# Kernel tuning notes

Hardware: AMD Instinct MI355X
Metric: run time of the kernel (lower is better)

Reference implementation:

```python
import jax, jax.numpy as jnp
import numpy as np

INPUT_NDIMS = 1024
HIDDEN = 512
LATENT = 50
BATCH = 16384

def setup_inputs() -> dict:
    key = jax.random.key(0)
    ks = jax.random.split(key, 12)
    s = 0.02
    x = jax.random.uniform(ks[0], (BATCH, INPUT_NDIMS), dtype=jnp.float32)
    u = 0.01 + 0.98 * jax.random.uniform(ks[1], (BATCH, LATENT), dtype=jnp.float32)
    W1 = s * jax.random.normal(ks[2], (HIDDEN, INPUT_NDIMS), dtype=jnp.float32)
    b1 = jnp.zeros((HIDDEN,), jnp.float32)
    Wa = s * jax.random.normal(ks[3], (LATENT, HIDDEN), dtype=jnp.float32)
    ba = jnp.zeros((LATENT,), jnp.float32)
    Wb = s * jax.random.normal(ks[4], (LATENT, HIDDEN), dtype=jnp.float32)
    bb = jnp.zeros((LATENT,), jnp.float32)
    W2 = s * jax.random.normal(ks[5], (HIDDEN, LATENT), dtype=jnp.float32)
    b2 = jnp.zeros((HIDDEN,), jnp.float32)
    W3 = s * jax.random.normal(ks[6], (INPUT_NDIMS, HIDDEN), dtype=jnp.float32)
    b3 = jnp.zeros((INPUT_NDIMS,), jnp.float32)
    return dict(x=x, u=u, W1=W1, b1=b1, Wa=Wa, ba=ba, Wb=Wb, bb=bb, W2=W2, b2=b2, W3=W3, b3=b3)

def _stick_segments(v):
    # pi[:, k] = v[:, k] * prod_{j<k} (1 - v[:, j])  -- single O(K) cumprod pass
    cp = jnp.cumprod(1.0 - v, axis=1)                       # inclusive cumprod
    excl = jnp.concatenate([jnp.ones_like(cp[:, :1]), cp[:, :-1]], axis=1)
    return v * excl

def reference(x, u, W1, b1, Wa, ba, Wb, bb, W2, b2, W3, b3):
    # encoder: MLP -> positive Kumaraswamy params alpha (param1), beta (param2)
    h = jax.nn.relu(x @ W1.T + b1)                           # [B, H]
    alpha = jax.nn.softplus(h @ Wa.T + ba) + 1e-4            # [B, K]
    beta = jax.nn.softplus(h @ Wb.T + bb) + 1e-4             # [B, K]
    # Kumaraswamy reparameterized sample: v = (1 - u^(1/beta))^(1/alpha)
    v = jnp.power(1.0 - jnp.power(u, 1.0 / beta), 1.0 / alpha)
    # set_v_K_to_one: force last stick fraction to 1 so segments sum to 1
    v = v.at[:, -1].set(1.0)
    pi = _stick_segments(v)                                  # [B, K], rows sum to 1
    # decoder: MLP with sigmoid output
    h2 = jax.nn.relu(pi @ W2.T + b2)                         # [B, H]
    recon = jax.nn.sigmoid(h2 @ W3.T + b3)                   # [B, D]
    return recon, alpha, beta
```

## Files before the change

### kernel.cpp

```cpp
#include <hip/hip_runtime.h>
#include <hip/hip_bf16.h>

typedef __hip_bfloat16 bf16_t;
typedef __attribute__((ext_vector_type(4))) float f32x4;
typedef __attribute__((ext_vector_type(8))) __bf16 bf16x8;
typedef __attribute__((ext_vector_type(8))) short s16x8;
typedef __attribute__((ext_vector_type(4))) unsigned short u16x4;

#define BATCH 16384
#define NDIM  1024
#define HID   512
#define LAT   50

#define LOG2E 1.44269504088896340736f
#define RLOG2E 0.69314718055994530942f

__device__ __forceinline__ float ex2(float x) { return __builtin_amdgcn_exp2f(x); }
__device__ __forceinline__ float lg2(float x) { return __builtin_amdgcn_logf(x); }
__device__ __forceinline__ float rcp(float x) { return __builtin_amdgcn_rcpf(x); }

__device__ inline unsigned short f2b_u(float f) {
  union { bf16_t b; unsigned short u; } cv; cv.b = __float2bfloat16(f); return cv.u;
}

__device__ __forceinline__ void gload16(const void* src, void* dst_lds) {
  __builtin_amdgcn_global_load_lds(
      reinterpret_cast<const __attribute__((address_space(1))) void*>(
          reinterpret_cast<unsigned long long>(src)),
      reinterpret_cast<__attribute__((address_space(3))) void*>(
          static_cast<unsigned>(reinterpret_cast<unsigned long long>(dst_lds))),
      16, 0, 0);
}

#define WAIT_VMCNT(N)                                          \
  do {                                                         \
    asm volatile("s_waitcnt vmcnt(%0)" ::"i"(N) : "memory");   \
    __builtin_amdgcn_sched_barrier(0);                         \
  } while (0)
#define WAIT_LGKM0                                             \
  do {                                                         \
    asm volatile("s_waitcnt lgkmcnt(0)" ::: "memory");         \
    __builtin_amdgcn_sched_barrier(0);                         \
  } while (0)

__global__ void prep_w_kernel(const float* __restrict__ W1, const float* __restrict__ W3,
                              const float* __restrict__ Wa, const float* __restrict__ Wb,
                              const float* __restrict__ W2, const float* __restrict__ ba,
                              const float* __restrict__ bb,
                              bf16_t* __restrict__ w1, bf16_t* __restrict__ w3,
                              bf16_t* __restrict__ wab, bf16_t* __restrict__ w2p,
                              float* __restrict__ bab)
{
  const int W1U  = (HID * NDIM) / 4;
  const int W3U  = (NDIM * HID) / 4;
  const int WABN = 128 * HID;
  const int W2PN = HID * 64;
  const int TOT  = W1U + W3U + WABN + W2PN + 128;
  for (int i = blockIdx.x * blockDim.x + threadIdx.x; i < TOT;
       i += gridDim.x * blockDim.x) {
    int j = i;
    if (j < W1U) {
      const f32x4 v = ((const f32x4*)W1)[j];
      u16x4 o; o[0]=f2b_u(v[0]); o[1]=f2b_u(v[1]); o[2]=f2b_u(v[2]); o[3]=f2b_u(v[3]);
      ((u16x4*)w1)[j] = o; continue;
    }
    j -= W1U;
    if (j < W3U) {
      const f32x4 v = ((const f32x4*)W3)[j];
      u16x4 o; o[0]=f2b_u(v[0]); o[1]=f2b_u(v[1]); o[2]=f2b_u(v[2]); o[3]=f2b_u(v[3]);
      ((u16x4*)w3)[j] = o; continue;
    }
    j -= W3U;
    if (j < WABN) {
      const int n = j >> 9, k = j & 511;
      float v = (n < 50) ? Wa[n * 512 + k] : ((n < 100) ? Wb[(n - 50) * 512 + k] : 0.f);
      wab[j] = __float2bfloat16(v); continue;
    }
    j -= WABN;
    if (j < W2PN) {
      const int n = j >> 6, k = j & 63;
      w2p[j] = __float2bfloat16(k < 50 ? W2[n * 50 + k] : 0.f); continue;
    }
    j -= W2PN;
    bab[j] = (j < 50) ? ba[j] : ((j < 100) ? bb[j - 50] : 0.f);
  }
}

template<int A_F32, int EPI, int BM>
__global__ __launch_bounds__(512, 2)
void gemm8p_kernel(const void* __restrict__ Av, const bf16_t* __restrict__ B,
                   const float* __restrict__ bias, void* __restrict__ out0,
                   int M, int N, int K)
{
  constexpr int BN     = 256;
  constexpr int ABYTES = BM * 128;
  constexpr int BUF    = ABYTES + BN * 128;
  constexpr int MI     = BM / 32;
  constexpr int FPQ    = MI / 4;
  constexpr int RA     = BM / 64;
  constexpr int RB     = 4;
  __shared__ char lds[2 * BUF];

  const int tid  = threadIdx.x;
  const int swzid = ((blockIdx.x & 7) * (gridDim.x >> 3)) + (blockIdx.x >> 3);
  const int nblocks = N / BN;
  const int bn   = swzid % nblocks;
  const int bm   = swzid / nblocks;
  const int wid  = tid >> 6;
  const int lane = tid & 63;
  const int l15  = lane & 15;
  const int l4   = lane >> 4;
  const int wm   = (wid >> 2) * (BM / 2);
  const int wn   = (wid & 3) * 64;
  const int uw   = __builtin_amdgcn_readfirstlane(wid);

  f32x4 acc[MI][4] = {};
  f32x4 areg[4];

  auto stage_A_round = [&](char* buf, int k0, int i) {
    const bf16_t* A = (const bf16_t*)Av;
    const int c  = (i * 8 + uw) * 64 + lane;
    const int r  = c >> 3;
    const int sp = c & 7;
    const int sl = sp ^ (r & 7);
    gload16(A + (size_t)(bm * BM + r) * K + k0 + sl * 8,
            buf + (i * 8 + uw) * 1024);
  };
  auto stage_B_round = [&](char* buf, int k0, int i) {
    char* lB = buf + ABYTES;
    const int c  = (i * 8 + uw) * 64 + lane;
    const int r  = c >> 3;
    const int sp = c & 7;
    const int sl = sp ^ (r & 7);
    gload16(B + (size_t)(bn * BN + r) * K + k0 + sl * 8,
            lB + (i * 8 + uw) * 1024);
  };
  auto load_A_f32 = [&](int k0) {
    const float* A = (const float*)Av;
    #pragma unroll
    for (int j = 0; j < 2; ++j) {
      const int c  = j * 512 + tid;
      const int r  = c >> 3;
      const int sl = c & 7;
      const float* s = A + (size_t)(bm * BM + r) * K + k0 + sl * 8;
      areg[2 * j]     = *(const f32x4*)s;
      areg[2 * j + 1] = *(const f32x4*)(s + 4);
    }
  };
  auto write_A_f32 = [&](char* buf) {
    #pragma unroll
    for (int j = 0; j < 2; ++j) {
      const int c  = j * 512 + tid;
      const int r  = c >> 3;
      const int sl = c & 7;
      const int sp = sl ^ (r & 7);
      union { s16x8 v; unsigned short us[8]; } o;
      const f32x4 v0 = areg[2 * j], v1 = areg[2 * j + 1];
      o.us[0]=f2b_u(v0[0]); o.us[1]=f2b_u(v0[1]); o.us[2]=f2b_u(v0[2]); o.us[3]=f2b_u(v0[3]);
      o.us[4]=f2b_u(v1[0]); o.us[5]=f2b_u(v1[1]); o.us[6]=f2b_u(v1[2]); o.us[7]=f2b_u(v1[3]);
      *(s16x8*)(buf + r * 128 + sp * 16) = o.v;
    }
  };

  const int nt = K >> 6;
  if constexpr (A_F32) {
    load_A_f32(0); write_A_f32(lds);
  } else {
    #pragma unroll
    for (int i = 0; i < RA; ++i) stage_A_round(lds, 0, i);
  }
  #pragma unroll
  for (int i = 0; i < RB; ++i) stage_B_round(lds, 0, i);
  WAIT_VMCNT(0);
  if (A_F32) WAIT_LGKM0;
  __builtin_amdgcn_s_barrier();

  for (int t = 0; t < nt; ++t) {
    char* buf  = lds + (t & 1) * BUF;
    char* nbuf = lds + ((t + 1) & 1) * BUF;
    const char* lA = buf;
    const char* lB = buf + ABYTES;
    const bool pf  = (t + 1 < nt);
    const int k0n  = (t + 1) << 6;

    if (A_F32 && pf) load_A_f32(k0n);

    #pragma unroll
    for (int q = 0; q < 4; ++q) {
      if (pf) {
        if constexpr (A_F32) {
          stage_B_round(nbuf, k0n, q);
        } else {
          if (q < RA) stage_A_round(nbuf, k0n, q);
          stage_B_round(nbuf, k0n, q);
        }
      }
      bf16x8 af[FPQ][2], bfr[4][2];
      #pragma unroll
      for (int f = 0; f < FPQ; ++f)
        #pragma unroll
        for (int h = 0; h < 2; ++h) {
          const int row = wm + (q * FPQ + f) * 16 + l15;
          const int sp  = (h * 4 + l4) ^ (row & 7);
          af[f][h] = *(const bf16x8*)(lA + row * 128 + sp * 16);
        }
      #pragma unroll
      for (int ni = 0; ni < 4; ++ni)
        #pragma unroll
        for (int h = 0; h < 2; ++h) {
          const int row = wn + ni * 16 + l15;
          const int sp  = (h * 4 + l4) ^ (row & 7);
          bfr[ni][h] = *(const bf16x8*)(lB + row * 128 + sp * 16);
        }
      __builtin_amdgcn_s_barrier();
      WAIT_LGKM0;
      __builtin_amdgcn_s_setprio(1);
      #pragma unroll
      for (int f = 0; f < FPQ; ++f)
        #pragma unroll
        for (int ni = 0; ni < 4; ++ni)
          #pragma unroll
          for (int h = 0; h < 2; ++h)
            acc[q * FPQ + f][ni] = __builtin_amdgcn_mfma_f32_16x16x32_bf16(
                af[f][h], bfr[ni][h], acc[q * FPQ + f][ni], 0, 0, 0);
      __builtin_amdgcn_s_setprio(0);
      if (q < 3) __builtin_amdgcn_s_barrier();
    }

    if (A_F32 && pf) write_A_f32(nbuf);
    WAIT_VMCNT(0);
    if (A_F32) WAIT_LGKM0;
    __builtin_amdgcn_s_barrier();
  }

  #pragma unroll
  for (int ni = 0; ni < 4; ++ni) {
    const int n  = bn * BN + wn + ni * 16 + l15;
    const float bv = bias[n];
    #pragma unroll
    for (int mi = 0; mi < MI; ++mi) {
      #pragma unroll
      for (int r = 0; r < 4; ++r) {
        const int m  = bm * BM + wm + mi * 16 + l4 * 4 + r;
        const float t = acc[mi][ni][r] + bv;
        if (EPI == 0) {
          ((bf16_t*)out0)[(size_t)m * N + n] = __float2bfloat16(fmaxf(t, 0.f));
        } else {
          ((float*)out0)[(size_t)m * N + n] = rcp(1.f + ex2(-t * LOG2E));
        }
      }
    }
  }
}

__global__ __launch_bounds__(512, 2)
void abstick_kernel(const bf16_t* __restrict__ A, const bf16_t* __restrict__ wabg,
                    const float* __restrict__ bab, const bf16_t* __restrict__ w2pg,
                    const float* __restrict__ b2, const float* __restrict__ u,
                    float* __restrict__ out_a, float* __restrict__ out_b,
                    bf16_t* __restrict__ h2)
{
  constexpr int BUF = 64 * 128 + 16384;
  constexpr int PIL = 65536;
  constexpr int SMO = 73728;
  __shared__ char lds[100352];

  const int tid  = threadIdx.x;
  const int swzid = ((blockIdx.x & 7) * (gridDim.x >> 3)) + (blockIdx.x >> 3);
  const int bm   = swzid;
  const int wid  = tid >> 6;
  const int lane = tid & 63;
  const int l15  = lane & 15;
  const int l4   = lane >> 4;
  const int wm   = (wid >> 2) * 32;
  const int wn   = (wid & 3) * 32;
  const int uw   = __builtin_amdgcn_readfirstlane(wid);
  const int K    = HID;

  f32x4 acc[2][2] = {};

  auto stage_AB = [&](char* buf, int k0) {
    {
      const int c  = tid;
      const int r  = c >> 3;
      const int sp = c & 7;
      const int sl = sp ^ (r & 7);
      gload16(A + (size_t)(bm * 64 + r) * K + k0 + sl * 8, buf + uw * 1024);
    }
    char* lB = buf + 8192;
    #pragma unroll
    for (int i = 0; i < 2; ++i) {
      const int c  = (i * 8 + uw) * 64 + lane;
      const int r  = c >> 3;
      const int sp = c & 7;
      const int sl = sp ^ (r & 7);
      gload16(wabg + (size_t)r * K + k0 + sl * 8, lB + (i * 8 + uw) * 1024);
    }
  };
  auto compute1 = [&](const char* buf) {
    const char* lA = buf;
    const char* lB = buf + 8192;
    #pragma unroll
    for (int h = 0; h < 2; ++h) {
      bf16x8 af[2], bfr[2];
      #pragma unroll
      for (int mi = 0; mi < 2; ++mi) {
        const int row = wm + mi * 16 + l15;
        const int sp  = (h * 4 + l4) ^ (row & 7);
        af[mi] = *(const bf16x8*)(lA + row * 128 + sp * 16);
      }
      #pragma unroll
      for (int ni = 0; ni < 2; ++ni) {
        const int row = wn + ni * 16 + l15;
        const int sp  = (h * 4 + l4) ^ (row & 7);
        bfr[ni] = *(const bf16x8*)(lB + row * 128 + sp * 16);
      }
      #pragma unroll
      for (int mi = 0; mi < 2; ++mi)
        #pragma unroll
        for (int ni = 0; ni < 2; ++ni)
          acc[mi][ni] = __builtin_amdgcn_mfma_f32_16x16x32_bf16(
              af[mi], bfr[ni], acc[mi][ni], 0, 0, 0);
    }
  };

  stage_AB(lds, 0);
  stage_AB(lds + BUF, 64);
  for (int t = 0; t < 8; ++t) {
    if (t + 1 < 8) WAIT_VMCNT(3);
    else           WAIT_VMCNT(0);
    __builtin_amdgcn_s_barrier();
    compute1(lds + (t & 1) * BUF);
    __builtin_amdgcn_s_barrier();
    __builtin_amdgcn_sched_barrier(0);
    if (t + 2 < 8) stage_AB(lds + (t & 1) * BUF, (t + 2) << 6);
  }

  #pragma unroll
  for (int i = 0; i < 8; ++i) {
    const int c  = (i * 8 + uw) * 64 + lane;
    const int r  = c >> 3;
    const int sp = c & 7;
    const int sl = sp ^ (r & 7);
    gload16(w2pg + (size_t)r * 64 + sl * 8, lds + (i * 8 + uw) * 1024);
  }

  float* sm = (float*)(lds + SMO);
  #pragma unroll
  for (int ni = 0; ni < 2; ++ni) {
    const int n  = wn + ni * 16 + l15;
    const float bv = bab[n];
    #pragma unroll
    for (int mi = 0; mi < 2; ++mi) {
      #pragma unroll
      for (int r = 0; r < 4; ++r) {
        const int ml = wm + mi * 16 + l4 * 4 + r;
        const int m  = bm * 64 + ml;
        const float t = acc[mi][ni][r] + bv;
        if (n < 100) {
          const float y =
              (t > 20.f ? t : lg2(1.f + ex2(t * LOG2E)) * RLOG2E) + 1e-4f;
          if (n < 50) out_a[(size_t)m * 50 + n] = y;
          else        out_b[(size_t)m * 50 + (n - 50)] = y;
          sm[ml * 104 + n + (n < 50 ? 0 : 2)] = y;
        }
      }
    }
  }
  __syncthreads();

  #pragma unroll 1
  for (int rr = 0; rr < 8; ++rr) {
    const int rl = wid * 8 + rr;
    const size_t m = (size_t)(bm * 64 + rl);
    float v = 1.f, t = 1.f;
    if (lane < 49) {
      const float a  = sm[rl * 104 + lane];
      const float b  = sm[rl * 104 + 52 + lane];
      const float uu = u[m * 50 + lane];
      const float tb = ex2(lg2(uu) * rcp(b));
      v = ex2(lg2(1.f - tb) * rcp(a));
      t = 1.f - v;
    }
    float p = t;
    #pragma unroll
    for (int d = 1; d < 64; d <<= 1) {
      const float o = __shfl_up(p, d, 64);
      if (lane >= d) p *= o;
    }
    float e = __shfl_up(p, 1, 64);
    if (lane == 0) e = 1.f;
    const float piv = (lane < 50) ? v * e : 0.f;
    *(unsigned short*)(lds + PIL + rl * 128 +
                       (((lane >> 3) ^ (rl & 7)) << 4) + ((lane & 7) << 1)) =
        f2b_u(piv);
  }
  __syncthreads();

  const int wn3 = (wid & 3) * 128;
  f32x4 acc3[2][8] = {};
  #pragma unroll
  for (int h = 0; h < 2; ++h) {
    bf16x8 af[2], bfr[8];
    #pragma unroll
    for (int mi = 0; mi < 2; ++mi) {
      const int row = wm + mi * 16 + l15;
      const int sp  = (h * 4 + l4) ^ (row & 7);
      af[mi] = *(const bf16x8*)(lds + PIL + row * 128 + sp * 16);
    }
    #pragma unroll
    for (int ni = 0; ni < 8; ++ni) {
      const int row = wn3 + ni * 16 + l15;
      const int sp  = (h * 4 + l4) ^ (row & 7);
      bfr[ni] = *(const bf16x8*)(lds + row * 128 + sp * 16);
    }
    #pragma unroll
    for (int mi = 0; mi < 2; ++mi)
      #pragma unroll
      for (int ni = 0; ni < 8; ++ni)
        acc3[mi][ni] = __builtin_amdgcn_mfma_f32_16x16x32_bf16(
            af[mi], bfr[ni], acc3[mi][ni], 0, 0, 0);
  }
  #pragma unroll
  for (int ni = 0; ni < 8; ++ni) {
    const int n  = wn3 + ni * 16 + l15;
    const float bv = b2[n];
    #pragma unroll
    for (int mi = 0; mi < 2; ++mi) {
      #pragma unroll
      for (int r = 0; r < 4; ++r) {
        const int m  = bm * 64 + wm + mi * 16 + l4 * 4 + r;
        h2[(size_t)m * HID + n] =
            __float2bfloat16(fmaxf(acc3[mi][ni][r] + bv, 0.f));
      }
    }
  }
}

extern "C" void kernel_launch(void* const* d_in, const int* in_sizes, int n_in,
                              void* d_out, int out_size, void* d_ws, size_t ws_size,
                              hipStream_t stream)
{
  const float* x  = (const float*)d_in[0];
  const float* u  = (const float*)d_in[1];
  const float* W1 = (const float*)d_in[2];
  const float* b1 = (const float*)d_in[3];
  const float* Wa = (const float*)d_in[4];
  const float* ba = (const float*)d_in[5];
  const float* Wb = (const float*)d_in[6];
  const float* bb = (const float*)d_in[7];
  const float* W2 = (const float*)d_in[8];
  const float* b2 = (const float*)d_in[9];
  const float* W3 = (const float*)d_in[10];
  const float* b3 = (const float*)d_in[11];

  float* recon  = (float*)d_out;
  float* oalpha = recon + (size_t)BATCH * NDIM;
  float* obeta  = oalpha + (size_t)BATCH * LAT;

  char* ws = (char*)d_ws;
  bf16_t* h2  = (bf16_t*)(ws);
  bf16_t* h   = (bf16_t*)(ws + 16777216);
  bf16_t* w1  = (bf16_t*)(ws + 33554432);
  bf16_t* w3  = (bf16_t*)(ws + 34603008);
  bf16_t* wab = (bf16_t*)(ws + 35651584);
  bf16_t* w2p = (bf16_t*)(ws + 35782656);
  float*  bab = (float*)(ws + 35848192);

  prep_w_kernel<<<512, 256, 0, stream>>>(W1, W3, Wa, Wb, W2, ba, bb,
                                         w1, w3, wab, w2p, bab);
  gemm8p_kernel<1, 0, 128><<<256, 512, 0, stream>>>(
      x, w1, b1, (void*)h, BATCH, HID, NDIM);
  abstick_kernel<<<256, 512, 0, stream>>>(
      h, wab, bab, w2p, b2, u, oalpha, obeta, h2);
  gemm8p_kernel<0, 1, 256><<<256, 512, 0, stream>>>(
      h2, w3, b3, (void*)recon, BATCH, NDIM, HID);
}
```

Measured before the change: 86.60 us.

## Triple-buffer GEMM LDS pipeline, drop intra-tile barriers, fix BM at 128

Both GEMMs now use a three-stage LDS ring that prefetches two k-tiles ahead and waits on a partial vmcnt instead of draining all loads each step. The per-quarter workgroup barriers go away, and B fragments are loaded once per k-tile and reused across the four A sub-tiles. The decoder GEMM now uses BM=128 with twice as many blocks. Launch bounds drop to one block per CU because LDS grows to three buffers, which costs occupancy in exchange for deeper memory latency hiding.

```diff
diff --git a/kernel.cpp b/kernel.cpp
--- a/kernel.cpp
+++ b/kernel.cpp
@@ -86,20 +86,20 @@
   }
 }
 
-template<int A_F32, int EPI, int BM>
-__global__ __launch_bounds__(512, 2)
-void gemm8p_kernel(const void* __restrict__ Av, const bf16_t* __restrict__ B,
+template<int A_F32, int EPI>
+__global__ __launch_bounds__(512, 1)
+void gemm3b_kernel(const void* __restrict__ Av, const bf16_t* __restrict__ B,
                    const float* __restrict__ bias, void* __restrict__ out0,
                    int M, int N, int K)
 {
+  constexpr int BM     = 128;
   constexpr int BN     = 256;
   constexpr int ABYTES = BM * 128;
   constexpr int BUF    = ABYTES + BN * 128;
-  constexpr int MI     = BM / 32;
-  constexpr int FPQ    = MI / 4;
-  constexpr int RA     = BM / 64;
+  constexpr int RA     = 2;
   constexpr int RB     = 4;
-  __shared__ char lds[2 * BUF];
+  constexpr int L      = A_F32 ? RB : (RA + RB);
+  __shared__ char lds[3 * BUF];
 
   const int tid  = threadIdx.x;
   const int swzid = ((blockIdx.x & 7) * (gridDim.x >> 3)) + (blockIdx.x >> 3);
@@ -110,11 +110,11 @@
   const int lane = tid & 63;
   const int l15  = lane & 15;
   const int l4   = lane >> 4;
-  const int wm   = (wid >> 2) * (BM / 2);
+  const int wm   = (wid >> 2) * 64;
   const int wn   = (wid & 3) * 64;
   const int uw   = __builtin_amdgcn_readfirstlane(wid);
 
-  f32x4 acc[MI][4] = {};
+  f32x4 acc[4][4] = {};
   f32x4 areg[4];
 
   auto stage_A_round = [&](char* buf, int k0, int i) {
@@ -171,64 +171,71 @@
   }
   #pragma unroll
   for (int i = 0; i < RB; ++i) stage_B_round(lds, 0, i);
-  WAIT_VMCNT(0);
+  if (nt > 1) {
+    if constexpr (!A_F32) {
+      #pragma unroll
+      for (int i = 0; i < RA; ++i) stage_A_round(lds + BUF, 64, i);
+    }
+    #pragma unroll
+    for (int i = 0; i < RB; ++i) stage_B_round(lds + BUF, 64, i);
+  }
+  WAIT_VMCNT(L);
   if (A_F32) WAIT_LGKM0;
   __builtin_amdgcn_s_barrier();
 
   for (int t = 0; t < nt; ++t) {
-    char* buf  = lds + (t & 1) * BUF;
-    char* nbuf = lds + ((t + 1) & 1) * BUF;
+    char* buf   = lds + (t % 3) * BUF;
+    char* buf1  = lds + ((t + 1) % 3) * BUF;
+    char* buf2  = lds + ((t + 2) % 3) * BUF;
     const char* lA = buf;
     const char* lB = buf + ABYTES;
-    const bool pf  = (t + 1 < nt);
-    const int k0n  = (t + 1) << 6;
-
-    if (A_F32 && pf) load_A_f32(k0n);
+    const bool pf1 = (t + 1 < nt);
+    const bool pf2 = (t + 2 < nt);
+    const int k0n2 = (t + 2) << 6;
+
+    if (A_F32 && pf1) load_A_f32((t + 1) << 6);
+
+    bf16x8 bfr[4][2];
+    #pragma unroll
+    for (int ni = 0; ni < 4; ++ni)
+      #pragma unroll
+      for (int h = 0; h < 2; ++h) {
+        const int row = wn + ni * 16 + l15;
+        const int sp  = (h * 4 + l4) ^ (row & 7);
+        bfr[ni][h] = *(const bf16x8*)(lB + row * 128 + sp * 16);
+      }
 
     #pragma unroll
     for (int q = 0; q < 4; ++q) {
-      if (pf) {
+      if (pf2) {
         if constexpr (A_F32) {
-          stage_B_round(nbuf, k0n, q);
+          stage_B_round(buf2, k0n2, q);
         } else {
-          if (q < RA) stage_A_round(nbuf, k0n, q);
-          stage_B_round(nbuf, k0n, q);
+          if (q < RA) stage_A_round(buf2, k0n2, q);
+          stage_B_round(buf2, k0n2, q);
         }
       }
-      bf16x8 af[FPQ][2], bfr[4][2];
-      #pragma unroll
-      for (int f = 0; f < FPQ; ++f)
-        #pragma unroll
-        for (int h = 0; h < 2; ++h) {
-          const int row = wm + (q * FPQ + f) * 16 + l15;
-          const int sp  = (h * 4 + l4) ^ (row & 7);
-          af[f][h] = *(const bf16x8*)(lA + row * 128 + sp * 16);
-        }
+      bf16x8 af[2];
+      #pragma unroll
+      for (int h = 0; h < 2; ++h) {
+        const int row = wm + q * 16 + l15;
+        const int sp  = (h * 4 + l4) ^ (row & 7);
+        af[h] = *(const bf16x8*)(lA + row * 128 + sp * 16);
+      }
+      WAIT_LGKM0;
+      __builtin_amdgcn_s_setprio(1);
       #pragma unroll
       for (int ni = 0; ni < 4; ++ni)
         #pragma unroll
-        for (int h = 0; h < 2; ++h) {
-          const int row = wn + ni * 16 + l15;
-          const int sp  = (h * 4 + l4) ^ (row & 7);
-          bfr[ni][h] = *(const bf16x8*)(lB + row * 128 + sp * 16);
-        }
-      __builtin_amdgcn_s_barrier();
-      WAIT_LGKM0;
-      __builtin_amdgcn_s_setprio(1);
-      #pragma unroll
-      for (int f = 0; f < FPQ; ++f)
-        #pragma unroll
-        for (int ni = 0; ni < 4; ++ni)
-          #pragma unroll
-          for (int h = 0; h < 2; ++h)
-            acc[q * FPQ + f][ni] = __builtin_amdgcn_mfma_f32_16x16x32_bf16(
-                af[f][h], bfr[ni][h], acc[q * FPQ + f][ni], 0, 0, 0);
+        for (int h = 0; h < 2; ++h)
+          acc[q][ni] = __builtin_amdgcn_mfma_f32_16x16x32_bf16(
+              af[h], bfr[ni][h], acc[q][ni], 0, 0, 0);
       __builtin_amdgcn_s_setprio(0);
-      if (q < 3) __builtin_amdgcn_s_barrier();
-    }
-
-    if (A_F32 && pf) write_A_f32(nbuf);
-    WAIT_VMCNT(0);
+    }
+
+    if (A_F32 && pf1) write_A_f32(buf1);
+    if (pf2) { WAIT_VMCNT(L); }
+    else     { WAIT_VMCNT(0); }
     if (A_F32) WAIT_LGKM0;
     __builtin_amdgcn_s_barrier();
   }
@@ -238,7 +245,7 @@
     const int n  = bn * BN + wn + ni * 16 + l15;
     const float bv = bias[n];
     #pragma unroll
-    for (int mi = 0; mi < MI; ++mi) {
+    for (int mi = 0; mi < 4; ++mi) {
       #pragma unroll
       for (int r = 0; r < 4; ++r) {
         const int m  = bm * BM + wm + mi * 16 + l4 * 4 + r;
@@ -469,10 +476,10 @@
 
   prep_w_kernel<<<512, 256, 0, stream>>>(W1, W3, Wa, Wb, W2, ba, bb,
                                          w1, w3, wab, w2p, bab);
-  gemm8p_kernel<1, 0, 128><<<256, 512, 0, stream>>>(
+  gemm3b_kernel<1, 0><<<256, 512, 0, stream>>>(
       x, w1, b1, (void*)h, BATCH, HID, NDIM);
   abstick_kernel<<<256, 512, 0, stream>>>(
       h, wab, bab, w2p, b2, u, oalpha, obeta, h2);
-  gemm8p_kernel<0, 1, 256><<<256, 512, 0, stream>>>(
+  gemm3b_kernel<0, 1><<<512, 512, 0, stream>>>(
       h2, w3, b3, (void*)recon, BATCH, NDIM, HID);
 }
```

New measurement: 82.86 us. 4.3% less time.
